# Kernel tuning notes

Hardware: AMD Instinct MI355X
Metric: run time of the kernel (lower is better)

## Reference

```python
import jax, jax.numpy as jnp
import numpy as np

B, S, H = 2, 2048, 1024
NUM_HEADS = 16


def setup_inputs() -> dict:
    key = jax.random.key(0)
    ks = jax.random.split(key, 5)
    scale = 1.0 / np.sqrt(H)
    x = jax.random.normal(ks[0], (B, S, H), dtype=jnp.float32)
    W_qkv = jax.random.normal(ks[1], (3 * H, H), dtype=jnp.float32) * scale
    b_qkv = jax.random.normal(ks[2], (3 * H,), dtype=jnp.float32) * 0.02
    W_o = jax.random.normal(ks[3], (H, H), dtype=jnp.float32) * scale
    b_o = jax.random.normal(ks[4], (H,), dtype=jnp.float32) * 0.02
    return {"x": x, "W_qkv": W_qkv, "b_qkv": b_qkv, "W_o": W_o, "b_o": b_o}


def reference(x, W_qkv, b_qkv, W_o, b_o):
    b, s, h = x.shape
    n = NUM_HEADS
    d_head = h // n
    # QKV projection (torch Linear: x @ W.T + b), then chunk into Q, K, V
    qkv = x @ W_qkv.T + b_qkv                      # [b, s, 3h]
    Q, K, V = jnp.split(qkv, 3, axis=-1)           # each [b, s, h]
    # split heads: b s (n d) -> b n s d
    Q = Q.reshape(b, s, n, d_head).transpose(0, 2, 1, 3)
    K = K.reshape(b, s, n, d_head).transpose(0, 2, 1, 3)
    V = V.reshape(b, s, n, d_head).transpose(0, 2, 1, 3)
    # scores, causal mask, scale (mask before/after scale is equivalent: -inf stays -inf)
    scores = jnp.einsum('bnqd,bnkd->bnqk', Q, K) / jnp.sqrt(jnp.float32(d_head))
    causal = jnp.tril(jnp.ones((s, s), dtype=bool))  # True = keep
    scores = jnp.where(causal, scores, -jnp.inf)
    A = jax.nn.softmax(scores, axis=-1)
    AV = jnp.einsum('bnqk,bnkd->bnqd', A, V)
    out = AV.transpose(0, 2, 1, 3).reshape(b, s, h)  # merge heads
    return out @ W_o.T + b_o
```

## Files before the change

kernel.cpp:

```cpp
#include <hip/hip_runtime.h>
#include <cstdint>
#include <cstddef>

#define BATCH 2
#define SEQ   2048
#define HID   1024
#define NHEAD 16
#define DHEAD 64
#define QKV_N 3072
#define NTOK  4096

typedef __attribute__((ext_vector_type(4))) float f32x4;
typedef __attribute__((ext_vector_type(8))) short bf16x8;

#define QSCL 0.18033688011112042f

__device__ inline unsigned short f2bf(float f) {
    union { float f; unsigned int u; } v; v.f = f;
    unsigned int u = v.u;
    unsigned int r = (u + 0x7fffu + ((u >> 16) & 1u)) >> 16;
    return (unsigned short)r;
}

__device__ __forceinline__ void gload_lds16(const void* g, void* l) {
    __builtin_amdgcn_global_load_lds(
        (const __attribute__((address_space(1))) void*)g,
        (__attribute__((address_space(3))) void*)l, 16, 0, 0);
}

__global__ void cast_f32_bf16(const float* __restrict__ in, unsigned short* __restrict__ out, int n4) {
    int i = blockIdx.x * blockDim.x + threadIdx.x;
    if (i >= n4) return;
    float4 v = reinterpret_cast<const float4*>(in)[i];
    ushort4 o;
    o.x = f2bf(v.x); o.y = f2bf(v.y); o.z = f2bf(v.z); o.w = f2bf(v.w);
    reinterpret_cast<ushort4*>(out)[i] = o;
}

template<int BN, int OUT_MODE>
__global__ __launch_bounds__(256) void gemm_bt(const short* __restrict__ A,
                                               const short* __restrict__ B,
                                               const float* __restrict__ bias,
                                               void* __restrict__ Cout,
                                               int M, int N, int K) {
    constexpr int WTN = BN / 2;
    constexpr int NJ  = WTN / 16;
    constexpr int NBC = BN / 64;

    __shared__ short sA[2][128 * 32];
    __shared__ short sB[2][BN * 32];

    const int tid  = threadIdx.x;
    const int lane = tid & 63;
    const int wave = tid >> 6;
    const int wm = wave >> 1, wn = wave & 1;

    const int nwg = gridDim.x;
    const int swz = (blockIdx.x & 7) * (nwg >> 3) + (blockIdx.x >> 3);
    const int tiles_n = N / BN;
    const int m0 = (swz / tiles_n) * 128;
    const int n0 = (swz % tiles_n) * BN;

    f32x4 acc[4][NJ];
    #pragma unroll
    for (int i = 0; i < 4; ++i)
        #pragma unroll
        for (int j = 0; j < NJ; ++j) acc[i][j] = (f32x4){0.f, 0.f, 0.f, 0.f};

    const int r = lane & 15;
    const int G = lane >> 4;

    #define GSTAGE(kt_, buf_)                                                          \
        {                                                                              \
            _Pragma("unroll")                                                          \
            for (int i = 0; i < 2; ++i) {                                              \
                int ga = (i * 4 + wave) * 64 + lane;                                   \
                int row = ga >> 2, gcol = (ga & 3) ^ (row & 3);                        \
                gload_lds16(A + (size_t)(m0 + row) * K + (kt_) + gcol * 8,             \
                            &sA[buf_][(i * 4 + wave) * 512]);                          \
            }                                                                          \
            _Pragma("unroll")                                                          \
            for (int i = 0; i < NBC; ++i) {                                            \
                int gb = (i * 4 + wave) * 64 + lane;                                   \
                int row = gb >> 2, gcol = (gb & 3) ^ (row & 3);                        \
                gload_lds16(B + (size_t)(n0 + row) * K + (kt_) + gcol * 8,             \
                            &sB[buf_][(i * 4 + wave) * 512]);                          \
            }                                                                          \
        }

    GSTAGE(0, 0);
    __syncthreads();
    int cur = 0;

    const int nsteps = K >> 5;
    for (int ks = 0; ks < nsteps; ++ks) {
        if (ks + 1 < nsteps) GSTAGE((ks + 1) * 32, cur ^ 1);

        const int sg = G ^ (r & 3);
        bf16x8 af[4], bfr[NJ];
        #pragma unroll
        for (int i = 0; i < 4; ++i) {
            int row = wm * 64 + i * 16 + r;
            af[i] = *reinterpret_cast<const bf16x8*>(&sA[cur][row * 32 + sg * 8]);
        }
        #pragma unroll
        for (int j = 0; j < NJ; ++j) {
            int row = wn * WTN + j * 16 + r;
            bfr[j] = *reinterpret_cast<const bf16x8*>(&sB[cur][row * 32 + sg * 8]);
        }
        #pragma unroll
        for (int i = 0; i < 4; ++i)
            #pragma unroll
            for (int j = 0; j < NJ; ++j)
                acc[i][j] = __builtin_amdgcn_mfma_f32_16x16x32_bf16(af[i], bfr[j], acc[i][j], 0, 0, 0);

        __syncthreads();
        cur ^= 1;
    }
    #undef GSTAGE

    const int col_l = lane & 15;
    const int row_g = (lane >> 4) * 4;
    #pragma unroll
    for (int i = 0; i < 4; ++i) {
        #pragma unroll
        for (int j = 0; j < NJ; ++j) {
            int nn = n0 + wn * WTN + j * 16 + col_l;
            float bv = bias[nn];
            float scl = (OUT_MODE == 2 && nn < HID) ? QSCL : 1.0f;
            #pragma unroll
            for (int reg = 0; reg < 4; ++reg) {
                int mm = m0 + wm * 64 + i * 16 + row_g + reg;
                float v = (acc[i][j][reg] + bv) * scl;
                if (OUT_MODE == 0) {
                    reinterpret_cast<float*>(Cout)[(size_t)mm * N + nn] = v;
                } else {
                    reinterpret_cast<unsigned short*>(Cout)[(size_t)mm * N + nn] = f2bf(v);
                }
            }
        }
    }
}

#define TLDP 72
__global__ __launch_bounds__(256) void transpose_v(const short* __restrict__ qkv,
                                                   short* __restrict__ vT) {
    const int st = blockIdx.x;
    const int bh = blockIdx.y;
    const int b  = bh >> 4, h = bh & 15;
    __shared__ short ld[64 * TLDP];
    const int tid = threadIdx.x;

    #pragma unroll
    for (int i = 0; i < 2; ++i) {
        int idx = i * 256 + tid;
        int row = idx >> 3, c = idx & 7;
        int4 v = *reinterpret_cast<const int4*>(
            qkv + ((size_t)(b * SEQ + st * 64 + row)) * QKV_N + 2 * HID + h * DHEAD + c * 8);
        *reinterpret_cast<int4*>(&ld[row * TLDP + c * 8]) = v;
    }
    __syncthreads();
    #pragma unroll
    for (int i = 0; i < 4; ++i) {
        int idx = i * 256 + tid;
        int d = idx >> 4, sc = idx & 15;
        ushort4 o;
        o.x = (unsigned short)ld[(sc * 4 + 0) * TLDP + d];
        o.y = (unsigned short)ld[(sc * 4 + 1) * TLDP + d];
        o.z = (unsigned short)ld[(sc * 4 + 2) * TLDP + d];
        o.w = (unsigned short)ld[(sc * 4 + 3) * TLDP + d];
        *reinterpret_cast<ushort4*>(&vT[((size_t)(bh * DHEAD + d)) * SEQ + st * 64 + sc * 4]) = o;
    }
}

#define SWZ(g_, row_) ((g_) ^ ((row_) & 7))

__global__ __launch_bounds__(128, 2) void attn_fwd(const short* __restrict__ qkv,
                                                   const short* __restrict__ vT,
                                                   short* __restrict__ av) {
    const int bh = blockIdx.y;
    const int b  = bh >> 4;
    const int h  = bh & 15;
    const int qt = (31 - blockIdx.x + blockIdx.y) & 31;

    __shared__ short sK [2][64 * 64];
    __shared__ short sVT[2][64 * 64];
    __shared__ short sP [2][32 * 64];

    const int tid  = threadIdx.x;
    const int lane = tid & 63;
    const int wave = tid >> 6;
    const int r    = lane & 15;
    const int G    = lane >> 4;
    const int row_g = G * 4;

    const int qbw = qt * 64 + wave * 32;

    bf16x8 qf[2][2];
    #pragma unroll
    for (int mi = 0; mi < 2; ++mi) {
        const short* Qg = qkv + ((size_t)(b * SEQ + qbw + mi * 16 + r)) * QKV_N + h * DHEAD;
        qf[mi][0] = *reinterpret_cast<const bf16x8*>(Qg + G * 8);
        qf[mi][1] = *reinterpret_cast<const bf16x8*>(Qg + 32 + G * 8);
    }

    f32x4 oacc[2][4];
    f32x4 oL[2];
    #pragma unroll
    for (int mi = 0; mi < 2; ++mi) {
        oL[mi] = (f32x4){0.f, 0.f, 0.f, 0.f};
        #pragma unroll
        for (int dg = 0; dg < 4; ++dg) oacc[mi][dg] = (f32x4){0.f, 0.f, 0.f, 0.f};
    }

    bf16x8 ones;
    #pragma unroll
    for (int e = 0; e < 8; ++e) ones[e] = (short)0x3f80;

    const int lrow = lane >> 3;
    const int lsg  = lane & 7;

    #define STAGE(kv0_, buf_)                                                              \
        {                                                                                  \
            _Pragma("unroll")                                                              \
            for (int i = 0; i < 4; ++i) {                                                  \
                int row  = i * 16 + wave * 8 + lrow;                                       \
                int srcg = lsg ^ (row & 7);                                                \
                gload_lds16(qkv + (size_t)(b * SEQ + (kv0_) + row) * QKV_N                 \
                                + HID + h * DHEAD + srcg * 8,                              \
                            &sK[buf_][(i * 128 + wave * 64) * 8]);                         \
                gload_lds16(vT + (size_t)(bh * DHEAD + row) * SEQ + (kv0_) + srcg * 8,     \
                            &sVT[buf_][(i * 128 + wave * 64) * 8]);                        \
            }                                                                              \
        }

    STAGE(0, 0);
    __syncthreads();
    int cur = 0;

    for (int t = 0; t <= qt; ++t) {
        if (t < qt) STAGE((t + 1) * 64, cur ^ 1);

        bf16x8 kb[4][2];
        #pragma unroll
        for (int g = 0; g < 4; ++g) {
            int row = g * 16 + r;
            kb[g][0] = *reinterpret_cast<const bf16x8*>(&sK[cur][row * 64 + SWZ(G, row) * 8]);
            kb[g][1] = *reinterpret_cast<const bf16x8*>(&sK[cur][row * 64 + SWZ(4 + G, row) * 8]);
        }

        const bool diag = (t == qt);

        #pragma unroll
        for (int mi = 0; mi < 2; ++mi) {
            f32x4 s[4];
            #pragma unroll
            for (int g = 0; g < 4; ++g) {
                f32x4 z = (f32x4){0.f, 0.f, 0.f, 0.f};
                z = __builtin_amdgcn_mfma_f32_16x16x32_bf16(qf[mi][0], kb[g][0], z, 0, 0, 0);
                z = __builtin_amdgcn_mfma_f32_16x16x32_bf16(qf[mi][1], kb[g][1], z, 0, 0, 0);
                s[g] = z;
            }
            if (diag) {
                #pragma unroll
                for (int g = 0; g < 4; ++g) {
                    #pragma unroll
                    for (int reg = 0; reg < 4; ++reg) {
                        int kvg = g * 16 + r;
                        int qg  = wave * 32 + mi * 16 + row_g + reg;
                        if (kvg > qg) s[g][reg] = -30000.f;
                    }
                }
            }
            #pragma unroll
            for (int g = 0; g < 4; ++g) {
                int gc = g * 2 + (r >> 3);
                #pragma unroll
                for (int reg = 0; reg < 4; ++reg) {
                    float p = __builtin_amdgcn_exp2f(s[g][reg]);
                    int row = mi * 16 + row_g + reg;
                    sP[wave][row * 64 + SWZ(gc, row) * 8 + (r & 7)] = (short)f2bf(p);
                }
            }
        }

        asm volatile("s_waitcnt lgkmcnt(0)" ::: "memory");
        __builtin_amdgcn_sched_barrier(0);

        bf16x8 vb[4][2];
        #pragma unroll
        for (int dg = 0; dg < 4; ++dg) {
            int row = dg * 16 + r;
            vb[dg][0] = *reinterpret_cast<const bf16x8*>(&sVT[cur][row * 64 + SWZ(G, row) * 8]);
            vb[dg][1] = *reinterpret_cast<const bf16x8*>(&sVT[cur][row * 64 + SWZ(4 + G, row) * 8]);
        }

        #pragma unroll
        for (int mi = 0; mi < 2; ++mi) {
            int prow = mi * 16 + r;
            bf16x8 pa0 = *reinterpret_cast<const bf16x8*>(&sP[wave][prow * 64 + SWZ(G, prow) * 8]);
            bf16x8 pa1 = *reinterpret_cast<const bf16x8*>(&sP[wave][prow * 64 + SWZ(4 + G, prow) * 8]);
            #pragma unroll
            for (int dg = 0; dg < 4; ++dg) {
                oacc[mi][dg] = __builtin_amdgcn_mfma_f32_16x16x32_bf16(pa0, vb[dg][0], oacc[mi][dg], 0, 0, 0);
                oacc[mi][dg] = __builtin_amdgcn_mfma_f32_16x16x32_bf16(pa1, vb[dg][1], oacc[mi][dg], 0, 0, 0);
            }
            oL[mi] = __builtin_amdgcn_mfma_f32_16x16x32_bf16(pa0, ones, oL[mi], 0, 0, 0);
            oL[mi] = __builtin_amdgcn_mfma_f32_16x16x32_bf16(pa1, ones, oL[mi], 0, 0, 0);
        }

        __syncthreads();
        cur ^= 1;
    }

    #pragma unroll
    for (int mi = 0; mi < 2; ++mi) {
        float il[4];
        #pragma unroll
        for (int reg = 0; reg < 4; ++reg) il[reg] = 1.0f / oL[mi][reg];
        #pragma unroll
        for (int dg = 0; dg < 4; ++dg) {
            #pragma unroll
            for (int reg = 0; reg < 4; ++reg) {
                float v = oacc[mi][dg][reg] * il[reg];
                size_t tok = (size_t)(b * SEQ + qbw + mi * 16 + row_g + reg);
                av[tok * HID + h * DHEAD + dg * 16 + r] = (short)f2bf(v);
            }
        }
    }
}

extern "C" void kernel_launch(void* const* d_in, const int* in_sizes, int n_in,
                              void* d_out, int out_size, void* d_ws, size_t ws_size,
                              hipStream_t stream) {
    const float* x     = (const float*)d_in[0];
    const float* W_qkv = (const float*)d_in[1];
    const float* b_qkv = (const float*)d_in[2];
    const float* W_o   = (const float*)d_in[3];
    const float* b_o   = (const float*)d_in[4];
    float* out = (float*)d_out;

    const int n_x    = NTOK * HID;
    const int n_wqkv = QKV_N * HID;
    const int n_wo   = HID * HID;
    const int n_qkv  = NTOK * QKV_N;
    const int n_av   = NTOK * HID;

    short* xb    = (short*)d_ws;
    short* wqkvb = xb + n_x;
    short* wob   = wqkvb + n_wqkv;
    short* qkv   = wob + n_wo;
    short* av    = qkv + n_qkv;
    short* vT    = av + n_av;

    cast_f32_bf16<<<n_x / 1024,    256, 0, stream>>>(x,     (unsigned short*)xb,    n_x / 4);
    cast_f32_bf16<<<n_wqkv / 1024, 256, 0, stream>>>(W_qkv, (unsigned short*)wqkvb, n_wqkv / 4);
    cast_f32_bf16<<<n_wo / 1024,   256, 0, stream>>>(W_o,   (unsigned short*)wob,   n_wo / 4);

    gemm_bt<128, 2><<<(NTOK / 128) * (QKV_N / 128), 256, 0, stream>>>(
        xb, wqkvb, b_qkv, (void*)qkv, NTOK, QKV_N, HID);

    transpose_v<<<dim3(SEQ / 64, BATCH * NHEAD), 256, 0, stream>>>(qkv, vT);

    attn_fwd<<<dim3(32, 32), 128, 0, stream>>>(qkv, vT, av);

    gemm_bt<64, 0><<<(NTOK / 128) * (HID / 64), 256, 0, stream>>>(
        av, wob, b_o, (void*)out, NTOK, HID, HID);
}
```

Measured before the change: 128.7 us.

## Keep softmax probabilities in registers via transposed MFMA operand order

Swaps the MFMA operand order so S is computed transposed (K as A, Q as B). Each lane then holds a column of probabilities that maps directly onto the B-operand layout of the PV MFMA, so the LDS round-trip through sP, its waitcnt and its sched barrier are removed. V fragments are gathered from LDS with 8-byte reads to match the new k-ordering. The output is now written as 4-wide vector stores. The risk is that the k-index permutation between the P and V fragments must match exactly, and the V reads are narrower and may hit more bank conflicts.

```diff
diff --git a/kernel.cpp b/kernel.cpp
--- a/kernel.cpp
+++ b/kernel.cpp
@@ -185,7 +185,6 @@
 
     __shared__ short sK [2][64 * 64];
     __shared__ short sVT[2][64 * 64];
-    __shared__ short sP [2][32 * 64];
 
     const int tid  = threadIdx.x;
     const int lane = tid & 63;
@@ -248,6 +247,22 @@
             kb[g][0] = *reinterpret_cast<const bf16x8*>(&sK[cur][row * 64 + SWZ(G, row) * 8]);
             kb[g][1] = *reinterpret_cast<const bf16x8*>(&sK[cur][row * 64 + SWZ(4 + G, row) * 8]);
         }
+        bf16x8 vb[4][2];
+        #pragma unroll
+        for (int dg = 0; dg < 4; ++dg) {
+            int row_d = dg * 16 + r;
+            int rm = row_d & 7;
+            int eo = (G & 1) * 4;
+            #pragma unroll
+            for (int c = 0; c < 2; ++c) {
+                int glo = (c * 4 + (G >> 1)) ^ rm;
+                int ghi = (c * 4 + 2 + (G >> 1)) ^ rm;
+                uint2 lo = *reinterpret_cast<const uint2*>(&sVT[cur][row_d * 64 + glo * 8 + eo]);
+                uint2 hi = *reinterpret_cast<const uint2*>(&sVT[cur][row_d * 64 + ghi * 8 + eo]);
+                int4 f; f.x = lo.x; f.y = lo.y; f.z = hi.x; f.w = hi.y;
+                __builtin_memcpy(&vb[dg][c], &f, 16);
+            }
+        }
 
         const bool diag = (t == qt);
 
@@ -257,56 +272,45 @@
             #pragma unroll
             for (int g = 0; g < 4; ++g) {
                 f32x4 z = (f32x4){0.f, 0.f, 0.f, 0.f};
-                z = __builtin_amdgcn_mfma_f32_16x16x32_bf16(qf[mi][0], kb[g][0], z, 0, 0, 0);
-                z = __builtin_amdgcn_mfma_f32_16x16x32_bf16(qf[mi][1], kb[g][1], z, 0, 0, 0);
+                z = __builtin_amdgcn_mfma_f32_16x16x32_bf16(kb[g][0], qf[mi][0], z, 0, 0, 0);
+                z = __builtin_amdgcn_mfma_f32_16x16x32_bf16(kb[g][1], qf[mi][1], z, 0, 0, 0);
                 s[g] = z;
             }
             if (diag) {
+                int qg = wave * 32 + mi * 16 + r;
                 #pragma unroll
                 for (int g = 0; g < 4; ++g) {
                     #pragma unroll
                     for (int reg = 0; reg < 4; ++reg) {
-                        int kvg = g * 16 + r;
-                        int qg  = wave * 32 + mi * 16 + row_g + reg;
+                        int kvg = g * 16 + row_g + reg;
                         if (kvg > qg) s[g][reg] = -30000.f;
                     }
                 }
             }
-            #pragma unroll
-            for (int g = 0; g < 4; ++g) {
-                int gc = g * 2 + (r >> 3);
+            bf16x8 pb[2];
+            #pragma unroll
+            for (int c = 0; c < 2; ++c) {
+                unsigned int w[4];
                 #pragma unroll
-                for (int reg = 0; reg < 4; ++reg) {
-                    float p = __builtin_amdgcn_exp2f(s[g][reg]);
-                    int row = mi * 16 + row_g + reg;
-                    sP[wave][row * 64 + SWZ(gc, row) * 8 + (r & 7)] = (short)f2bf(p);
+                for (int hh = 0; hh < 2; ++hh) {
+                    float p0 = __builtin_amdgcn_exp2f(s[2 * c + hh][0]);
+                    float p1 = __builtin_amdgcn_exp2f(s[2 * c + hh][1]);
+                    float p2 = __builtin_amdgcn_exp2f(s[2 * c + hh][2]);
+                    float p3 = __builtin_amdgcn_exp2f(s[2 * c + hh][3]);
+                    w[hh * 2 + 0] = (unsigned int)f2bf(p0) | ((unsigned int)f2bf(p1) << 16);
+                    w[hh * 2 + 1] = (unsigned int)f2bf(p2) | ((unsigned int)f2bf(p3) << 16);
                 }
-            }
-        }
-
-        asm volatile("s_waitcnt lgkmcnt(0)" ::: "memory");
-        __builtin_amdgcn_sched_barrier(0);
-
-        bf16x8 vb[4][2];
-        #pragma unroll
-        for (int dg = 0; dg < 4; ++dg) {
-            int row = dg * 16 + r;
-            vb[dg][0] = *reinterpret_cast<const bf16x8*>(&sVT[cur][row * 64 + SWZ(G, row) * 8]);
-            vb[dg][1] = *reinterpret_cast<const bf16x8*>(&sVT[cur][row * 64 + SWZ(4 + G, row) * 8]);
-        }
-
-        #pragma unroll
-        for (int mi = 0; mi < 2; ++mi) {
-            int prow = mi * 16 + r;
-            bf16x8 pa0 = *reinterpret_cast<const bf16x8*>(&sP[wave][prow * 64 + SWZ(G, prow) * 8]);
-            bf16x8 pa1 = *reinterpret_cast<const bf16x8*>(&sP[wave][prow * 64 + SWZ(4 + G, prow) * 8]);
+                int4 f; f.x = (int)w[0]; f.y = (int)w[1]; f.z = (int)w[2]; f.w = (int)w[3];
+                __builtin_memcpy(&pb[c], &f, 16);
+            }
+
             #pragma unroll
             for (int dg = 0; dg < 4; ++dg) {
-                oacc[mi][dg] = __builtin_amdgcn_mfma_f32_16x16x32_bf16(pa0, vb[dg][0], oacc[mi][dg], 0, 0, 0);
-                oacc[mi][dg] = __builtin_amdgcn_mfma_f32_16x16x32_bf16(pa1, vb[dg][1], oacc[mi][dg], 0, 0, 0);
-            }
-            oL[mi] = __builtin_amdgcn_mfma_f32_16x16x32_bf16(pa0, ones, oL[mi], 0, 0, 0);
-            oL[mi] = __builtin_amdgcn_mfma_f32_16x16x32_bf16(pa1, ones, oL[mi], 0, 0, 0);
+                oacc[mi][dg] = __builtin_amdgcn_mfma_f32_16x16x32_bf16(vb[dg][0], pb[0], oacc[mi][dg], 0, 0, 0);
+                oacc[mi][dg] = __builtin_amdgcn_mfma_f32_16x16x32_bf16(vb[dg][1], pb[1], oacc[mi][dg], 0, 0, 0);
+            }
+            oL[mi] = __builtin_amdgcn_mfma_f32_16x16x32_bf16(ones, pb[0], oL[mi], 0, 0, 0);
+            oL[mi] = __builtin_amdgcn_mfma_f32_16x16x32_bf16(ones, pb[1], oL[mi], 0, 0, 0);
         }
 
         __syncthreads();
@@ -315,17 +319,16 @@
 
     #pragma unroll
     for (int mi = 0; mi < 2; ++mi) {
-        float il[4];
-        #pragma unroll
-        for (int reg = 0; reg < 4; ++reg) il[reg] = 1.0f / oL[mi][reg];
+        float il = 1.0f / oL[mi][0];
+        size_t tok = (size_t)(b * SEQ + qbw + mi * 16 + r);
         #pragma unroll
         for (int dg = 0; dg < 4; ++dg) {
-            #pragma unroll
-            for (int reg = 0; reg < 4; ++reg) {
-                float v = oacc[mi][dg][reg] * il[reg];
-                size_t tok = (size_t)(b * SEQ + qbw + mi * 16 + row_g + reg);
-                av[tok * HID + h * DHEAD + dg * 16 + r] = (short)f2bf(v);
-            }
+            ushort4 o;
+            o.x = f2bf(oacc[mi][dg][0] * il);
+            o.y = f2bf(oacc[mi][dg][1] * il);
+            o.z = f2bf(oacc[mi][dg][2] * il);
+            o.w = f2bf(oacc[mi][dg][3] * il);
+            *reinterpret_cast<ushort4*>(&av[tok * HID + h * DHEAD + dg * 16 + row_g]) = o;
         }
     }
 }
```

Result: no change. 131.1 us (+1.8%).
